# Kernel optimization log

Hardware: AMD Instinct MI355X
Metric: run time of the kernel (lower is better)

## Reference

```python
import jax, jax.numpy as jnp
import numpy as np

B, M, K = 4096, 64, 3          # graphs, points per graph, knn k
FX, FP = 59, 3                 # node features, position dims (FX+FP = 62)
EPS = 1e-5


def _lin_init(key, fan_in, fan_out):
    k1, k2 = jax.random.split(key)
    s = 1.0 / np.sqrt(fan_in)
    W = jax.random.uniform(k1, (fan_in, fan_out), jnp.float32, -s, s)
    b = jax.random.uniform(k2, (fan_out,), jnp.float32, -s, s)
    return W, b


def setup_inputs() -> dict:
    key = jax.random.key(0)
    ks = jax.random.split(key, 8)
    x = jax.random.normal(ks[0], (B * M, FX), jnp.float32)
    pos = jax.random.normal(ks[1], (B * M, FP), jnp.float32)
    batch = jnp.repeat(jnp.arange(B, dtype=jnp.int32), M)
    W1, b1 = _lin_init(ks[2], FX + FP, 128)
    W2, b2 = _lin_init(ks[3], 128, 128)
    Wc1, bc1 = _lin_init(ks[4], 128, 256)
    Wc2, bc2 = _lin_init(ks[5], 256, 1)
    return dict(
        x=x, pos=pos, batch=batch,
        W1=W1, b1=b1, g1=jnp.ones(128), be1=jnp.zeros(128),
        W2=W2, b2=b2, g2=jnp.ones(128), be2=jnp.zeros(128),
        Wc1=Wc1, bc1=bc1, gc1=jnp.ones(256), bec1=jnp.zeros(256),
        Wc2=Wc2, bc2=bc2, gc2=jnp.ones(1), bec2=jnp.zeros(1),
    )


def _mlp_block(h, W, b, g, be):
    # Linear -> ReLU -> BatchNorm1d (training-mode batch statistics)
    h = jax.nn.relu(h @ W + b)
    mu = h.mean(axis=0)
    var = h.var(axis=0)  # biased, as torch BN uses for normalization
    return g * (h - mu) * jax.lax.rsqrt(var + EPS) + be


def _knn_idx(pos_b):
    # pos_b: [B, M, FP]; per-graph k-NN (loop=False)
    d = jnp.sum((pos_b[:, :, None, :] - pos_b[:, None, :, :]) ** 2, axis=-1)  # [B,M,M]
    d = d + jnp.eye(M, dtype=d.dtype) * 1e10  # exclude self-loops
    _, nbr = jax.lax.top_k(-d, K)  # [B, M, K] neighbor (source) indices
    return nbr


def reference(x, pos, batch, W1, b1, g1, be1, W2, b2, g2, be2,
              Wc1, bc1, gc1, bec1, Wc2, bc2, gc2, bec2):
    x_b = x.reshape(B, M, FX)
    pos_b = pos.reshape(B, M, FP)
    nbr = _knn_idx(pos_b)                                   # [B,M,K]
    # gather neighbor features and relative positions (edge messages)
    xj = jax.vmap(lambda xb, nb: xb[nb])(x_b, nbr)          # [B,M,K,FX]
    pj = jax.vmap(lambda pb, nb: pb[nb])(pos_b, nbr)        # [B,M,K,FP]
    rel = pj - pos_b[:, :, None, :]
    msg = jnp.concatenate([xj, rel], axis=-1).reshape(B * M * K, FX + FP)
    # local_nn on every edge, then max aggregation per target node
    h = _mlp_block(msg, W1, b1, g1, be1)                    # [E,128]
    h = h.reshape(B, M, K, 128).max(axis=2).reshape(B * M, 128)
    # global_nn per node
    h = _mlp_block(h, W2, b2, g2, be2)                      # [N,128]
    # global mean pool over graphs
    sums = jax.ops.segment_sum(h, batch, num_segments=B)
    cnt = jax.ops.segment_sum(jnp.ones((B * M,), h.dtype), batch, num_segments=B)
    pooled = sums / cnt[:, None]                            # [B,128]
    # classifier MLP([128,256,1])
    c = _mlp_block(pooled, Wc1, bc1, gc1, bec1)
    c = _mlp_block(c, Wc2, bc2, gc2, bec2)                  # [B,1]
    return jax.nn.sigmoid(c)[:, 0]
```

## Files before the change

### kernel.cpp

```cpp
#include <hip/hip_runtime.h>
#include <hip/hip_bf16.h>
#include <math.h>

#define NB   4096
#define MM   64
#define KNN  3
#define FX   59
#define H    128
#define NN   (NB*MM)
#define NE   (NN*KNN)
#define C1   256
#define EPSB 1e-5f

typedef __attribute__((ext_vector_type(8))) short short8;
typedef __attribute__((ext_vector_type(4))) float f32x4;

__device__ __forceinline__ float wave_red(float v) {
#pragma unroll
    for (int m = 32; m >= 1; m >>= 1) v += __shfl_xor(v, m, 64);
    return v;
}

__device__ __forceinline__ unsigned short f2bf(float f) {
    union { float f; unsigned u; } v; v.f = f;
    unsigned r = v.u + 0x7fffu + ((v.u >> 16) & 1u);
    return (unsigned short)(r >> 16);
}

__device__ __forceinline__ unsigned int pack_bf2(float a, float b) {
    union { __hip_bfloat162 h; unsigned int u; } cv;
    cv.h = __float22bfloat162_rn(make_float2(a, b));
    return cv.u;
}

__global__ __launch_bounds__(128) void k_prep2(
    const float* __restrict__ W2, const float* __restrict__ affine1,
    const float* __restrict__ b2, unsigned short* __restrict__ W2t,
    float* __restrict__ b2p)
{
    const int n = blockIdx.x, k = threadIdx.x;
    float wv = W2[k * H + n];
    W2t[n * H + k] = f2bf(affine1[k] * wv);
    float contrib = wave_red(affine1[H + k] * wv);
    __shared__ float red2[2];
    if ((k & 63) == 0) red2[k >> 6] = contrib;
    __syncthreads();
    if (k == 0) b2p[n] = b2[n] + red2[0] + red2[1];
}

__global__ __launch_bounds__(512, 8) void k_knn_mfma1(
    const float* __restrict__ x, const float* __restrict__ pos,
    const float* __restrict__ W1, const float* __restrict__ b1,
    unsigned short* __restrict__ h1max, float* __restrict__ p1s,
    float* __restrict__ p1q)
{
    __shared__ float pos_s[MM * 3];
    __shared__ int   nbr_s[MM * 3];
    __shared__ float b1_s[H];
    __shared__ float w1p_s[3 * H];
    __shared__ __align__(16) unsigned short a_s[MM * 72];
    __shared__ __align__(16) unsigned int   u_s32[MM * 66];

    const int blk = blockIdx.x, tid = threadIdx.x;
    const float* xg = x + (size_t)blk * MM * FX;
    const float* pg = pos + (size_t)blk * MM * 3;

    {
        const int node = tid >> 3, c0g = (tid & 7) * 8;
        unsigned short vals[8];
#pragma unroll
        for (int i = 0; i < 8; ++i) {
            int c = c0g + i;
            float v = (c < FX) ? xg[node * FX + c]
                               : ((c < 62) ? pg[node * 3 + (c - FX)] : 0.f);
            vals[i] = f2bf(v);
        }
        *(short8*)(a_s + node * 72 + c0g) = *(short8*)&vals[0];
    }
    if (tid < MM * 3) pos_s[tid] = pg[tid];
    if (tid < H) b1_s[tid] = b1[tid];
    if (tid < 3 * H) w1p_s[tid] = W1[(FX + (tid >> 7)) * H + (tid & 127)];

    const int lane = tid & 63;
    const int w    = tid >> 6;
    const int m    = lane & 15;
    const int kg   = lane >> 4;
    const int ch   = w * 16 + m;

    short8 bfr[2];
#pragma unroll
    for (int kc = 0; kc < 2; ++kc) {
        unsigned short t8[8];
#pragma unroll
        for (int i = 0; i < 8; ++i) {
            int k = kc * 32 + kg * 8 + i;
            t8[i] = (k < 62) ? f2bf(W1[k * H + ch]) : (unsigned short)0;
        }
        bfr[kc] = *(short8*)t8;
    }
    __syncthreads();

    {
        const int node = tid >> 3, q = tid & 7;
        const float px = pos_s[node * 3 + 0];
        const float py = pos_s[node * 3 + 1];
        const float pz = pos_s[node * 3 + 2];
        float d0 = 1e30f, d1 = 1e30f, d2 = 1e30f;
        int   i0 = 1 << 30, i1 = 1 << 30, i2 = 1 << 30;
        for (int jj = 0; jj < 8; ++jj) {
            int j = q * 8 + jj;
            if (j == node) continue;
            float dx = pos_s[j * 3 + 0] - px;
            float dy = pos_s[j * 3 + 1] - py;
            float dz = pos_s[j * 3 + 2] - pz;
            float d = dx * dx + dy * dy + dz * dz;
            bool b2v = (d < d2) || (d == d2 && j < i2);
            bool b1v = (d < d1) || (d == d1 && j < i1);
            bool b0v = (d < d0) || (d == d0 && j < i0);
            float nd2 = b1v ? d1 : d; int ni2 = b1v ? i1 : j;
            float nd1 = b0v ? d0 : d; int ni1 = b0v ? i0 : j;
            d2 = b2v ? nd2 : d2; i2 = b2v ? ni2 : i2;
            d1 = b1v ? nd1 : d1; i1 = b1v ? ni1 : i1;
            d0 = b0v ? d   : d0; i0 = b0v ? j   : i0;
        }
#pragma unroll
        for (int mq = 1; mq <= 4; mq <<= 1) {
            float e[3]; int f[3];
            e[0] = __shfl_xor(d0, mq, 64); f[0] = __shfl_xor(i0, mq, 64);
            e[1] = __shfl_xor(d1, mq, 64); f[1] = __shfl_xor(i1, mq, 64);
            e[2] = __shfl_xor(d2, mq, 64); f[2] = __shfl_xor(i2, mq, 64);
#pragma unroll
            for (int t3 = 0; t3 < 3; ++t3) {
                float ev = e[t3]; int fv = f[t3];
                bool b2v = (ev < d2) || (ev == d2 && fv < i2);
                bool b1v = (ev < d1) || (ev == d1 && fv < i1);
                bool b0v = (ev < d0) || (ev == d0 && fv < i0);
                float nd2 = b1v ? d1 : ev; int ni2 = b1v ? i1 : fv;
                float nd1 = b0v ? d0 : ev; int ni1 = b0v ? i0 : fv;
                d2 = b2v ? nd2 : d2; i2 = b2v ? ni2 : i2;
                d1 = b1v ? nd1 : d1; i1 = b1v ? ni1 : i1;
                d0 = b0v ? ev  : d0; i0 = b0v ? fv  : i0;
            }
        }
        if (q == 0) {
            nbr_s[node * 3 + 0] = i0;
            nbr_s[node * 3 + 1] = i1;
            nbr_s[node * 3 + 2] = i2;
        }
    }

    f32x4 acc[4];
#pragma unroll
    for (int rt = 0; rt < 4; ++rt) acc[rt] = (f32x4){0.f, 0.f, 0.f, 0.f};

#pragma unroll
    for (int kc = 0; kc < 2; ++kc)
#pragma unroll
        for (int rt = 0; rt < 4; ++rt) {
            short8 a = *(const short8*)(a_s + (rt * 16 + m) * 72 + kc * 32 + kg * 8);
            acc[rt] = __builtin_amdgcn_mfma_f32_16x16x32_bf16(bfr[kc], a, acc[rt], 0, 0, 0);
        }
#pragma unroll
    for (int rt = 0; rt < 4; ++rt) {
        int node = rt * 16 + m;
        int pidx = 8 * w + 2 * kg;
        uint2 val;
        val.x = pack_bf2(acc[rt][0], acc[rt][1]);
        val.y = pack_bf2(acc[rt][2], acc[rt][3]);
        *(uint2*)(u_s32 + node * 66 + pidx) = val;
    }
    __syncthreads();

    const int c0 = 2 * lane, c1v = 2 * lane + 1;
    const float wpa0 = w1p_s[c0],      wpa1 = w1p_s[H + c0],  wpa2 = w1p_s[2 * H + c0];
    const float wpb0 = w1p_s[c1v],     wpb1 = w1p_s[H + c1v], wpb2 = w1p_s[2 * H + c1v];
    const float b1a = b1_s[c0], b1b = b1_s[c1v];
    float s0 = 0.f, s1 = 0.f, q0 = 0.f, q1 = 0.f;
    unsigned int* hout32 = (unsigned int*)(h1max + (size_t)blk * MM * H);
#pragma unroll
    for (int ii = 0; ii < 8; ++ii) {
        int node = w * 8 + ii;
        int j0 = nbr_s[node * 3 + 0];
        int j1 = nbr_s[node * 3 + 1];
        int j2 = nbr_s[node * 3 + 2];
        float px = pos_s[node * 3 + 0], py = pos_s[node * 3 + 1], pz = pos_s[node * 3 + 2];
        float basea = b1a - (px * wpa0 + py * wpa1 + pz * wpa2);
        float baseb = b1b - (px * wpb0 + py * wpb1 + pz * wpb2);
        unsigned int v0 = u_s32[j0 * 66 + lane];
        unsigned int v1 = u_s32[j1 * 66 + lane];
        unsigned int v2 = u_s32[j2 * 66 + lane];
        float h0a = fmaxf(__uint_as_float(v0 << 16) + basea, 0.f);
        float h1a = fmaxf(__uint_as_float(v1 << 16) + basea, 0.f);
        float h2a = fmaxf(__uint_as_float(v2 << 16) + basea, 0.f);
        float h0b = fmaxf(__uint_as_float(v0 & 0xffff0000u) + baseb, 0.f);
        float h1b = fmaxf(__uint_as_float(v1 & 0xffff0000u) + baseb, 0.f);
        float h2b = fmaxf(__uint_as_float(v2 & 0xffff0000u) + baseb, 0.f);
        s0 += h0a + h1a + h2a; q0 += h0a * h0a + h1a * h1a + h2a * h2a;
        s1 += h0b + h1b + h2b; q1 += h0b * h0b + h1b * h1b + h2b * h2b;
        float ma = fmaxf(fmaxf(h0a, h1a), h2a);
        float mb = fmaxf(fmaxf(h0b, h1b), h2b);
        hout32[node * 64 + lane] = pack_bf2(ma, mb);
    }
    __syncthreads();

    float* s_red = (float*)a_s;
    float* q_red = (float*)u_s32;
    *(float2*)(s_red + w * 128 + c0) = make_float2(s0, s1);
    *(float2*)(q_red + w * 128 + c0) = make_float2(q0, q1);
    __syncthreads();
    if (tid < 128) {
        float S = 0.f;
#pragma unroll
        for (int ww = 0; ww < 8; ++ww) S += s_red[ww * 128 + tid];
        p1s[(size_t)blk * H + tid] = S;
    } else if (tid < 256) {
        int t2 = tid - 128;
        float Q = 0.f;
#pragma unroll
        for (int ww = 0; ww < 8; ++ww) Q += q_red[ww * 128 + t2];
        p1q[(size_t)blk * H + t2] = Q;
    }
}

__global__ __launch_bounds__(256) void k_stats(
    const float* __restrict__ ps, const float* __restrict__ pq, int P, int ld,
    float invCnt, const float* __restrict__ g, const float* __restrict__ be,
    float* __restrict__ affine, int C)
{
    const int c = blockIdx.x, tid = threadIdx.x;
    float s = 0.f, q = 0.f;
    for (int p = tid; p < P; p += 256) {
        s += ps[(size_t)p * ld + c];
        q += pq[(size_t)p * ld + c];
    }
    s = wave_red(s); q = wave_red(q);
    __shared__ float rs_s[4], rq_s[4];
    if ((tid & 63) == 0) { rs_s[tid >> 6] = s; rq_s[tid >> 6] = q; }
    __syncthreads();
    if (tid == 0) {
        float S = rs_s[0] + rs_s[1] + rs_s[2] + rs_s[3];
        float Q = rq_s[0] + rq_s[1] + rq_s[2] + rq_s[3];
        float mu  = S * invCnt;
        float var = Q * invCnt - mu * mu;
        float a   = g[c] * rsqrtf(var + EPSB);
        affine[c]     = a;
        affine[C + c] = be[c] - mu * a;
    }
}

__global__ __launch_bounds__(256) void k_mfma2(
    const unsigned short* __restrict__ h1max, const unsigned short* __restrict__ W2t,
    const float* __restrict__ b2p,
    float* __restrict__ graphsum, float* __restrict__ p2q)
{
    const int blk = blockIdx.x, tid = threadIdx.x;
    const unsigned short* hg = h1max + (size_t)blk * MM * H;
    const int lane = tid & 63, w = tid >> 6, wcol = w * 32;
    const int m = lane & 15, kg = lane >> 4;

    short8 bfr[2][4];
#pragma unroll
    for (int ct = 0; ct < 2; ++ct)
#pragma unroll
        for (int kc = 0; kc < 4; ++kc)
            bfr[ct][kc] = *(const short8*)(W2t + (wcol + ct * 16 + m) * H + kc * 32 + kg * 8);

    f32x4 acc[4][2];
#pragma unroll
    for (int rt = 0; rt < 4; ++rt)
#pragma unroll
        for (int ct = 0; ct < 2; ++ct) acc[rt][ct] = (f32x4){0.f, 0.f, 0.f, 0.f};

#pragma unroll
    for (int kc = 0; kc < 4; ++kc)
#pragma unroll
        for (int rt = 0; rt < 4; ++rt) {
            short8 a = *(const short8*)(hg + (rt * 16 + m) * H + kc * 32 + kg * 8);
#pragma unroll
            for (int ct = 0; ct < 2; ++ct)
                acc[rt][ct] = __builtin_amdgcn_mfma_f32_16x16x32_bf16(a, bfr[ct][kc], acc[rt][ct], 0, 0, 0);
        }

#pragma unroll
    for (int ct = 0; ct < 2; ++ct) {
        float bv = b2p[wcol + ct * 16 + m];
        float s = 0.f, q = 0.f;
#pragma unroll
        for (int rt = 0; rt < 4; ++rt)
#pragma unroll
            for (int r = 0; r < 4; ++r) {
                float v = fmaxf(acc[rt][ct][r] + bv, 0.f);
                s += v; q += v * v;
            }
        s += __shfl_xor(s, 16, 64); q += __shfl_xor(q, 16, 64);
        s += __shfl_xor(s, 32, 64); q += __shfl_xor(q, 32, 64);
        if (lane < 16) {
            int col = wcol + ct * 16 + lane;
            graphsum[(size_t)blk * H + col] = s;
            p2q[(size_t)blk * H + col] = q;
        }
    }
}

__global__ __launch_bounds__(256) void k_cls1(
    const float* __restrict__ graphsum, const float* __restrict__ affine2,
    const float* __restrict__ Wc1, const float* __restrict__ bc1,
    float* __restrict__ c1raw, float* __restrict__ p3s, float* __restrict__ p3q)
{
    __shared__ float pooled_s[16 * H];
    const int blk = blockIdx.x, tid = threadIdx.x;
    const int g0 = blk * 16;
    for (int t = tid; t < 16 * H; t += 256) {
        int f = t & 127;
        pooled_s[t] = affine2[f] * (graphsum[(size_t)g0 * H + t] * (1.f / 64.f)) + affine2[H + f];
    }
    __syncthreads();
    const int c = tid;
    float acc[16];
    const float bias = bc1[c];
#pragma unroll
    for (int gi = 0; gi < 16; ++gi) acc[gi] = bias;
    for (int f = 0; f < H; ++f) {
        float w = Wc1[f * C1 + c];
#pragma unroll
        for (int gi = 0; gi < 16; ++gi) acc[gi] += pooled_s[gi * H + f] * w;
    }
    float s = 0.f, q = 0.f;
#pragma unroll
    for (int gi = 0; gi < 16; ++gi) {
        float h = fmaxf(acc[gi], 0.f);
        c1raw[(size_t)(g0 + gi) * C1 + c] = h;
        s += h; q += h * h;
    }
    p3s[(size_t)blk * C1 + c] = s;
    p3q[(size_t)blk * C1 + c] = q;
}

__global__ __launch_bounds__(256) void k_cls2(
    const float* __restrict__ c1raw, const float* __restrict__ affine3,
    const float* __restrict__ Wc2, const float* __restrict__ bc2,
    float* __restrict__ z, float* __restrict__ pz, float* __restrict__ pzq)
{
    __shared__ float a_s[C1], c_s[C1], w_s[C1];
    const int blk = blockIdx.x, tid = threadIdx.x;
    a_s[tid] = affine3[tid];
    c_s[tid] = affine3[C1 + tid];
    w_s[tid] = Wc2[tid];
    __syncthreads();
    const int g = blk * 256 + tid;
    float acc = bc2[0];
    for (int f = 0; f < C1; f += 4) {
        float4 cv = *(const float4*)&c1raw[(size_t)g * C1 + f];
        acc += (a_s[f + 0] * cv.x + c_s[f + 0]) * w_s[f + 0];
        acc += (a_s[f + 1] * cv.y + c_s[f + 1]) * w_s[f + 1];
        acc += (a_s[f + 2] * cv.z + c_s[f + 2]) * w_s[f + 2];
        acc += (a_s[f + 3] * cv.w + c_s[f + 3]) * w_s[f + 3];
    }
    float zz = fmaxf(acc, 0.f);
    z[g] = zz;
    float s = wave_red(zz);
    float q = wave_red(zz * zz);
    __shared__ float rs_s[4], rq_s[4];
    if ((tid & 63) == 0) { rs_s[tid >> 6] = s; rq_s[tid >> 6] = q; }
    __syncthreads();
    if (tid == 0) {
        pz[blk]  = rs_s[0] + rs_s[1] + rs_s[2] + rs_s[3];
        pzq[blk] = rq_s[0] + rq_s[1] + rq_s[2] + rq_s[3];
    }
}

__global__ __launch_bounds__(256) void k_final(
    const float* __restrict__ z, const float* __restrict__ pz,
    const float* __restrict__ pzq, const float* __restrict__ gc2,
    const float* __restrict__ bec2, float* __restrict__ out)
{
    __shared__ float ab[2];
    if (threadIdx.x == 0) {
        float S = 0.f, Q = 0.f;
        for (int p = 0; p < 16; ++p) { S += pz[p]; Q += pzq[p]; }
        float mu  = S * (1.f / 4096.f);
        float var = Q * (1.f / 4096.f) - mu * mu;
        float a   = gc2[0] * rsqrtf(var + EPSB);
        ab[0] = a;
        ab[1] = bec2[0] - mu * a;
    }
    __syncthreads();
    float a = ab[0], cb = ab[1];
    for (int g = threadIdx.x; g < NB; g += 256) {
        float v = a * z[g] + cb;
        out[g] = 1.f / (1.f + expf(-v));
    }
}

extern "C" void kernel_launch(void* const* d_in, const int* in_sizes, int n_in,
                              void* d_out, int out_size, void* d_ws, size_t ws_size,
                              hipStream_t stream)
{
    const float* x    = (const float*)d_in[0];
    const float* pos  = (const float*)d_in[1];
    const float* W1   = (const float*)d_in[3];
    const float* b1   = (const float*)d_in[4];
    const float* g1   = (const float*)d_in[5];
    const float* be1  = (const float*)d_in[6];
    const float* W2   = (const float*)d_in[7];
    const float* b2   = (const float*)d_in[8];
    const float* g2   = (const float*)d_in[9];
    const float* be2  = (const float*)d_in[10];
    const float* Wc1  = (const float*)d_in[11];
    const float* bc1  = (const float*)d_in[12];
    const float* gc1  = (const float*)d_in[13];
    const float* bec1 = (const float*)d_in[14];
    const float* Wc2  = (const float*)d_in[15];
    const float* bc2  = (const float*)d_in[16];
    const float* gc2  = (const float*)d_in[17];
    const float* bec2 = (const float*)d_in[18];
    float* out = (float*)d_out;

    float* ws = (float*)d_ws;
    size_t off = 0;
    auto alloc = [&](size_t n) { float* p = ws + off; off += n; return p; };
    unsigned short* h1max = (unsigned short*)alloc((size_t)NN * H / 2);
    unsigned short* W2t   = (unsigned short*)alloc(128 * 128 / 2);
    float* b2p     = alloc(H);
    float* p1s     = alloc((size_t)NB * H);
    float* p1q     = alloc((size_t)NB * H);
    float* affine1 = alloc(2 * H);
    float* graphsum= alloc((size_t)NB * H);
    float* p2q     = alloc((size_t)NB * H);
    float* affine2 = alloc(2 * H);
    float* c1raw   = alloc((size_t)NB * C1);
    float* p3s     = alloc((size_t)256 * C1);
    float* p3q     = alloc((size_t)256 * C1);
    float* affine3 = alloc(2 * C1);
    float* zbuf    = alloc(NB);
    float* pz      = alloc(16);
    float* pzq     = alloc(16);

    k_knn_mfma1<<<dim3(NB), dim3(512), 0, stream>>>(x, pos, W1, b1, h1max, p1s, p1q);
    k_stats<<<dim3(H), dim3(256), 0, stream>>>(p1s, p1q, NB, H, 1.f / (float)NE, g1, be1, affine1, H);
    k_prep2<<<dim3(128), dim3(128), 0, stream>>>(W2, affine1, b2, W2t, b2p);
    k_mfma2<<<dim3(NB), dim3(256), 0, stream>>>(h1max, W2t, b2p, graphsum, p2q);
    k_stats<<<dim3(H), dim3(256), 0, stream>>>(graphsum, p2q, NB, H, 1.f / (float)NN, g2, be2, affine2, H);
    k_cls1<<<dim3(256), dim3(256), 0, stream>>>(graphsum, affine2, Wc1, bc1, c1raw, p3s, p3q);
    k_stats<<<dim3(C1), dim3(256), 0, stream>>>(p3s, p3q, 256, C1, 1.f / (float)NB, gc1, bec1, affine3, C1);
    k_cls2<<<dim3(16), dim3(256), 0, stream>>>(c1raw, affine3, Wc2, bc2, zbuf, pz, pzq);
    k_final<<<dim3(1), dim3(256), 0, stream>>>(zbuf, pz, pzq, gc2, bec2, out);
}
```

Measured before the change: 278.9 us.

## Fuse stats and classifier stages into cooperative kernels with grid sync

Replaces the chain of small kernels (stats, prep2, stats, cls1, stats, cls2, final) with two cooperative kernels that use grid-wide syncs between phases. Column statistics are now reduced by 256 blocks in parallel instead of one block per channel looping over 4096 partials. k_mfma2 also stages its A tile into padded LDS before the MFMA loop. This removes launch gaps and serial reductions, at the cost of grid-sync overhead and cooperative-launch constraints.

Result: slower. 380.9 us (+36.5%).

```diff
diff --git a/kernel.cpp b/kernel.cpp
--- a/kernel.cpp
+++ b/kernel.cpp
@@ -1,6 +1,9 @@
 #include <hip/hip_runtime.h>
 #include <hip/hip_bf16.h>
+#include <hip/hip_cooperative_groups.h>
 #include <math.h>
+
+namespace cg = cooperative_groups;
 
 #define NB   4096
 #define MM   64
@@ -31,21 +34,6 @@
     union { __hip_bfloat162 h; unsigned int u; } cv;
     cv.h = __float22bfloat162_rn(make_float2(a, b));
     return cv.u;
-}
-
-__global__ __launch_bounds__(128) void k_prep2(
-    const float* __restrict__ W2, const float* __restrict__ affine1,
-    const float* __restrict__ b2, unsigned short* __restrict__ W2t,
-    float* __restrict__ b2p)
-{
-    const int n = blockIdx.x, k = threadIdx.x;
-    float wv = W2[k * H + n];
-    W2t[n * H + k] = f2bf(affine1[k] * wv);
-    float contrib = wave_red(affine1[H + k] * wv);
-    __shared__ float red2[2];
-    if ((k & 63) == 0) red2[k >> 6] = contrib;
-    __syncthreads();
-    if (k == 0) b2p[n] = b2[n] + red2[0] + red2[1];
 }
 
 __global__ __launch_bounds__(512, 8) void k_knn_mfma1(
@@ -222,30 +210,59 @@
     }
 }
 
-__global__ __launch_bounds__(256) void k_stats(
-    const float* __restrict__ ps, const float* __restrict__ pq, int P, int ld,
-    float invCnt, const float* __restrict__ g, const float* __restrict__ be,
-    float* __restrict__ affine, int C)
+__global__ __launch_bounds__(256) void k_mid(
+    const float* __restrict__ p1s, const float* __restrict__ p1q,
+    const float* __restrict__ W2, const float* __restrict__ g1,
+    const float* __restrict__ be1, const float* __restrict__ b2,
+    float* __restrict__ pp1s, float* __restrict__ pp1q,
+    unsigned short* __restrict__ W2t, float* __restrict__ b2p)
 {
-    const int c = blockIdx.x, tid = threadIdx.x;
-    float s = 0.f, q = 0.f;
-    for (int p = tid; p < P; p += 256) {
-        s += ps[(size_t)p * ld + c];
-        q += pq[(size_t)p * ld + c];
-    }
-    s = wave_red(s); q = wave_red(q);
-    __shared__ float rs_s[4], rq_s[4];
-    if ((tid & 63) == 0) { rs_s[tid >> 6] = s; rq_s[tid >> 6] = q; }
-    __syncthreads();
-    if (tid == 0) {
-        float S = rs_s[0] + rs_s[1] + rs_s[2] + rs_s[3];
-        float Q = rq_s[0] + rq_s[1] + rq_s[2] + rq_s[3];
-        float mu  = S * invCnt;
-        float var = Q * invCnt - mu * mu;
-        float a   = g[c] * rsqrtf(var + EPSB);
-        affine[c]     = a;
-        affine[C + c] = be[c] - mu * a;
-    }
+    const int b = blockIdx.x, tid = threadIdx.x;
+    {
+        const int cgp = b & 7, pc = b >> 3;
+        const int m = tid & 15, r = tid >> 4;
+        const int c = cgp * 16 + m;
+        float s = 0.f, q = 0.f;
+#pragma unroll
+        for (int i = 0; i < 8; ++i) {
+            int p = pc * 128 + r + i * 16;
+            s += p1s[(size_t)p * H + c];
+            q += p1q[(size_t)p * H + c];
+        }
+        s += __shfl_xor(s, 16, 64); s += __shfl_xor(s, 32, 64);
+        q += __shfl_xor(q, 16, 64); q += __shfl_xor(q, 32, 64);
+        __shared__ float rs[4][16], rq[4][16];
+        const int w = tid >> 6, lane = tid & 63;
+        if (lane < 16) { rs[w][lane] = s; rq[w][lane] = q; }
+        __syncthreads();
+        if (tid < 16)
+            pp1s[pc * H + cgp * 16 + tid] = rs[0][tid] + rs[1][tid] + rs[2][tid] + rs[3][tid];
+        else if (tid < 32) {
+            int t = tid - 16;
+            pp1q[pc * H + cgp * 16 + t] = rq[0][t] + rq[1][t] + rq[2][t] + rq[3][t];
+        }
+    }
+    cg::this_grid().sync();
+    if (b >= H) return;
+    const int n = b, k = tid;
+    float contrib = 0.f;
+    if (k < H) {
+        float S = 0.f, Q = 0.f;
+#pragma unroll 8
+        for (int p = 0; p < 32; ++p) { S += pp1s[p * H + k]; Q += pp1q[p * H + k]; }
+        float mu  = S * (1.f / (float)NE);
+        float var = Q * (1.f / (float)NE) - mu * mu;
+        float a   = g1[k] * rsqrtf(var + EPSB);
+        float cc  = be1[k] - mu * a;
+        float wv  = W2[k * H + n];
+        W2t[n * H + k] = f2bf(a * wv);
+        contrib = cc * wv;
+    }
+    contrib = wave_red(contrib);
+    __shared__ float red2[4];
+    if ((tid & 63) == 0) red2[tid >> 6] = contrib;
+    __syncthreads();
+    if (tid == 0) b2p[n] = b2[n] + red2[0] + red2[1] + red2[2] + red2[3];
 }
 
 __global__ __launch_bounds__(256) void k_mfma2(
@@ -253,8 +270,15 @@
     const float* __restrict__ b2p,
     float* __restrict__ graphsum, float* __restrict__ p2q)
 {
+    __shared__ __align__(16) unsigned short a_s[MM * 136];
     const int blk = blockIdx.x, tid = threadIdx.x;
     const unsigned short* hg = h1max + (size_t)blk * MM * H;
+    for (int t = tid; t < MM * H / 8; t += 256) {
+        int row = t >> 4, col8 = (t & 15) * 8;
+        *(short8*)(a_s + row * 136 + col8) = *(const short8*)(hg + row * H + col8);
+    }
+    __syncthreads();
+
     const int lane = tid & 63, w = tid >> 6, wcol = w * 32;
     const int m = lane & 15, kg = lane >> 4;
 
@@ -275,7 +299,7 @@
     for (int kc = 0; kc < 4; ++kc)
 #pragma unroll
         for (int rt = 0; rt < 4; ++rt) {
-            short8 a = *(const short8*)(hg + (rt * 16 + m) * H + kc * 32 + kg * 8);
+            short8 a = *(const short8*)(a_s + (rt * 16 + m) * 136 + kc * 32 + kg * 8);
 #pragma unroll
             for (int ct = 0; ct < 2; ++ct)
                 acc[rt][ct] = __builtin_amdgcn_mfma_f32_16x16x32_bf16(a, bfr[ct][kc], acc[rt][ct], 0, 0, 0);
@@ -302,93 +326,160 @@
     }
 }
 
-__global__ __launch_bounds__(256) void k_cls1(
-    const float* __restrict__ graphsum, const float* __restrict__ affine2,
+__global__ __launch_bounds__(256) void k_tail(
+    const float* __restrict__ graphsum, const float* __restrict__ p2q,
+    const float* __restrict__ g2, const float* __restrict__ be2,
     const float* __restrict__ Wc1, const float* __restrict__ bc1,
-    float* __restrict__ c1raw, float* __restrict__ p3s, float* __restrict__ p3q)
+    const float* __restrict__ gc1, const float* __restrict__ bec1,
+    const float* __restrict__ Wc2, const float* __restrict__ bc2,
+    const float* __restrict__ gc2, const float* __restrict__ bec2,
+    float* __restrict__ pp2s, float* __restrict__ pp2q,
+    float* __restrict__ c1raw, float* __restrict__ p3s, float* __restrict__ p3q,
+    float* __restrict__ affine3, float* __restrict__ pzs, float* __restrict__ pzq,
+    float* __restrict__ out)
 {
+    const int b = blockIdx.x, tid = threadIdx.x;
+
+    {
+        const int cgp = b & 7, pc = b >> 3;
+        const int m = tid & 15, r = tid >> 4;
+        const int c = cgp * 16 + m;
+        float s = 0.f, q = 0.f;
+#pragma unroll
+        for (int i = 0; i < 8; ++i) {
+            int p = pc * 128 + r + i * 16;
+            s += graphsum[(size_t)p * H + c];
+            q += p2q[(size_t)p * H + c];
+        }
+        s += __shfl_xor(s, 16, 64); s += __shfl_xor(s, 32, 64);
+        q += __shfl_xor(q, 16, 64); q += __shfl_xor(q, 32, 64);
+        __shared__ float rs[4][16], rq[4][16];
+        const int w = tid >> 6, lane = tid & 63;
+        if (lane < 16) { rs[w][lane] = s; rq[w][lane] = q; }
+        __syncthreads();
+        if (tid < 16)
+            pp2s[pc * H + cgp * 16 + tid] = rs[0][tid] + rs[1][tid] + rs[2][tid] + rs[3][tid];
+        else if (tid < 32) {
+            int t = tid - 16;
+            pp2q[pc * H + cgp * 16 + t] = rq[0][t] + rq[1][t] + rq[2][t] + rq[3][t];
+        }
+    }
+    cg::this_grid().sync();
+
+    __shared__ float a2_s[H], c2_s[H];
+    if (tid < H) {
+        float S = 0.f, Q = 0.f;
+#pragma unroll 8
+        for (int p = 0; p < 32; ++p) { S += pp2s[p * H + tid]; Q += pp2q[p * H + tid]; }
+        float mu  = S * (1.f / (float)NN);
+        float var = Q * (1.f / (float)NN) - mu * mu;
+        float a   = g2[tid] * rsqrtf(var + EPSB);
+        a2_s[tid] = a;
+        c2_s[tid] = be2[tid] - mu * a;
+    }
+    __syncthreads();
     __shared__ float pooled_s[16 * H];
-    const int blk = blockIdx.x, tid = threadIdx.x;
-    const int g0 = blk * 16;
+    const int g0 = b * 16;
     for (int t = tid; t < 16 * H; t += 256) {
         int f = t & 127;
-        pooled_s[t] = affine2[f] * (graphsum[(size_t)g0 * H + t] * (1.f / 64.f)) + affine2[H + f];
-    }
-    __syncthreads();
-    const int c = tid;
-    float acc[16];
-    const float bias = bc1[c];
-#pragma unroll
-    for (int gi = 0; gi < 16; ++gi) acc[gi] = bias;
-    for (int f = 0; f < H; ++f) {
-        float w = Wc1[f * C1 + c];
-#pragma unroll
-        for (int gi = 0; gi < 16; ++gi) acc[gi] += pooled_s[gi * H + f] * w;
-    }
-    float s = 0.f, q = 0.f;
-#pragma unroll
-    for (int gi = 0; gi < 16; ++gi) {
-        float h = fmaxf(acc[gi], 0.f);
-        c1raw[(size_t)(g0 + gi) * C1 + c] = h;
-        s += h; q += h * h;
-    }
-    p3s[(size_t)blk * C1 + c] = s;
-    p3q[(size_t)blk * C1 + c] = q;
-}
-
-__global__ __launch_bounds__(256) void k_cls2(
-    const float* __restrict__ c1raw, const float* __restrict__ affine3,
-    const float* __restrict__ Wc2, const float* __restrict__ bc2,
-    float* __restrict__ z, float* __restrict__ pz, float* __restrict__ pzq)
-{
-    __shared__ float a_s[C1], c_s[C1], w_s[C1];
-    const int blk = blockIdx.x, tid = threadIdx.x;
-    a_s[tid] = affine3[tid];
-    c_s[tid] = affine3[C1 + tid];
-    w_s[tid] = Wc2[tid];
-    __syncthreads();
-    const int g = blk * 256 + tid;
-    float acc = bc2[0];
-    for (int f = 0; f < C1; f += 4) {
-        float4 cv = *(const float4*)&c1raw[(size_t)g * C1 + f];
-        acc += (a_s[f + 0] * cv.x + c_s[f + 0]) * w_s[f + 0];
-        acc += (a_s[f + 1] * cv.y + c_s[f + 1]) * w_s[f + 1];
-        acc += (a_s[f + 2] * cv.z + c_s[f + 2]) * w_s[f + 2];
-        acc += (a_s[f + 3] * cv.w + c_s[f + 3]) * w_s[f + 3];
-    }
-    float zz = fmaxf(acc, 0.f);
-    z[g] = zz;
-    float s = wave_red(zz);
-    float q = wave_red(zz * zz);
-    __shared__ float rs_s[4], rq_s[4];
-    if ((tid & 63) == 0) { rs_s[tid >> 6] = s; rq_s[tid >> 6] = q; }
+        pooled_s[t] = a2_s[f] * (graphsum[(size_t)g0 * H + t] * (1.f / 64.f)) + c2_s[f];
+    }
+    __syncthreads();
+    {
+        const int c = tid;
+        float acc[16];
+        const float bias = bc1[c];
+#pragma unroll
+        for (int gi = 0; gi < 16; ++gi) acc[gi] = bias;
+        for (int f = 0; f < H; ++f) {
+            float wv = Wc1[f * C1 + c];
+#pragma unroll
+            for (int gi = 0; gi < 16; ++gi) acc[gi] += pooled_s[gi * H + f] * wv;
+        }
+        float s = 0.f, q = 0.f;
+#pragma unroll
+        for (int gi = 0; gi < 16; ++gi) {
+            float h = fmaxf(acc[gi], 0.f);
+            c1raw[(size_t)(g0 + gi) * C1 + c] = h;
+            s += h; q += h * h;
+        }
+        p3s[(size_t)b * C1 + c] = s;
+        p3q[(size_t)b * C1 + c] = q;
+    }
+    cg::this_grid().sync();
+
+    {
+        float s = p3s[(size_t)tid * C1 + b];
+        float q = p3q[(size_t)tid * C1 + b];
+        s = wave_red(s); q = wave_red(q);
+        __shared__ float rs2[4], rq2[4];
+        if ((tid & 63) == 0) { rs2[tid >> 6] = s; rq2[tid >> 6] = q; }
+        __syncthreads();
+        if (tid == 0) {
+            float S = rs2[0] + rs2[1] + rs2[2] + rs2[3];
+            float Q = rq2[0] + rq2[1] + rq2[2] + rq2[3];
+            float mu  = S * (1.f / (float)NB);
+            float var = Q * (1.f / (float)NB) - mu * mu;
+            float a   = gc1[b] * rsqrtf(var + EPSB);
+            affine3[b]      = a;
+            affine3[C1 + b] = bec1[b] - mu * a;
+        }
+    }
+    cg::this_grid().sync();
+
+    __shared__ float a3_s[C1], c3_s[C1], w3_s[C1];
+    __shared__ float zloc[16];
+    a3_s[tid] = affine3[tid];
+    c3_s[tid] = affine3[C1 + tid];
+    w3_s[tid] = Wc2[tid];
+    __syncthreads();
+    {
+        const int gi = tid >> 4, part = tid & 15;
+        const int g = g0 + gi;
+        const float* crow = c1raw + (size_t)g * C1 + part * 16;
+        float acc3 = 0.f;
+#pragma unroll
+        for (int i = 0; i < 16; i += 4) {
+            float4 cv = *(const float4*)(crow + i);
+            int f = part * 16 + i;
+            acc3 += (a3_s[f + 0] * cv.x + c3_s[f + 0]) * w3_s[f + 0];
+            acc3 += (a3_s[f + 1] * cv.y + c3_s[f + 1]) * w3_s[f + 1];
+            acc3 += (a3_s[f + 2] * cv.z + c3_s[f + 2]) * w3_s[f + 2];
+            acc3 += (a3_s[f + 3] * cv.w + c3_s[f + 3]) * w3_s[f + 3];
+        }
+#pragma unroll
+        for (int mm = 1; mm <= 8; mm <<= 1) acc3 += __shfl_xor(acc3, mm, 64);
+        if (part == 0) zloc[gi] = fmaxf(acc3 + bc2[0], 0.f);
+    }
     __syncthreads();
     if (tid == 0) {
-        pz[blk]  = rs_s[0] + rs_s[1] + rs_s[2] + rs_s[3];
-        pzq[blk] = rq_s[0] + rq_s[1] + rq_s[2] + rq_s[3];
-    }
-}
-
-__global__ __launch_bounds__(256) void k_final(
-    const float* __restrict__ z, const float* __restrict__ pz,
-    const float* __restrict__ pzq, const float* __restrict__ gc2,
-    const float* __restrict__ bec2, float* __restrict__ out)
-{
-    __shared__ float ab[2];
-    if (threadIdx.x == 0) {
-        float S = 0.f, Q = 0.f;
-        for (int p = 0; p < 16; ++p) { S += pz[p]; Q += pzq[p]; }
-        float mu  = S * (1.f / 4096.f);
-        float var = Q * (1.f / 4096.f) - mu * mu;
-        float a   = gc2[0] * rsqrtf(var + EPSB);
-        ab[0] = a;
-        ab[1] = bec2[0] - mu * a;
-    }
-    __syncthreads();
-    float a = ab[0], cb = ab[1];
-    for (int g = threadIdx.x; g < NB; g += 256) {
-        float v = a * z[g] + cb;
-        out[g] = 1.f / (1.f + expf(-v));
+        float s = 0.f, q = 0.f;
+#pragma unroll
+        for (int i = 0; i < 16; ++i) { float z = zloc[i]; s += z; q += z * z; }
+        pzs[b] = s; pzq[b] = q;
+    }
+    cg::this_grid().sync();
+
+    {
+        float s = pzs[tid], q = pzq[tid];
+        s = wave_red(s); q = wave_red(q);
+        __shared__ float rs4[4], rq4[4], ab[2];
+        if ((tid & 63) == 0) { rs4[tid >> 6] = s; rq4[tid >> 6] = q; }
+        __syncthreads();
+        if (tid == 0) {
+            float S = rs4[0] + rs4[1] + rs4[2] + rs4[3];
+            float Q = rq4[0] + rq4[1] + rq4[2] + rq4[3];
+            float mu  = S * (1.f / (float)NB);
+            float var = Q * (1.f / (float)NB) - mu * mu;
+            float a   = gc2[0] * rsqrtf(var + EPSB);
+            ab[0] = a;
+            ab[1] = bec2[0] - mu * a;
+        }
+        __syncthreads();
+        if (tid < 16) {
+            float v = ab[0] * zloc[tid] + ab[1];
+            out[g0 + tid] = 1.f / (1.f + expf(-v));
+        }
     }
 }
 
@@ -424,25 +515,33 @@
     float* b2p     = alloc(H);
     float* p1s     = alloc((size_t)NB * H);
     float* p1q     = alloc((size_t)NB * H);
-    float* affine1 = alloc(2 * H);
+    float* pp1s    = alloc(32 * H);
+    float* pp1q    = alloc(32 * H);
     float* graphsum= alloc((size_t)NB * H);
     float* p2q     = alloc((size_t)NB * H);
-    float* affine2 = alloc(2 * H);
+    float* pp2s    = alloc(32 * H);
+    float* pp2q    = alloc(32 * H);
     float* c1raw   = alloc((size_t)NB * C1);
     float* p3s     = alloc((size_t)256 * C1);
     float* p3q     = alloc((size_t)256 * C1);
     float* affine3 = alloc(2 * C1);
-    float* zbuf    = alloc(NB);
-    float* pz      = alloc(16);
-    float* pzq     = alloc(16);
+    float* pzs     = alloc(256);
+    float* pzq     = alloc(256);
 
     k_knn_mfma1<<<dim3(NB), dim3(512), 0, stream>>>(x, pos, W1, b1, h1max, p1s, p1q);
-    k_stats<<<dim3(H), dim3(256), 0, stream>>>(p1s, p1q, NB, H, 1.f / (float)NE, g1, be1, affine1, H);
-    k_prep2<<<dim3(128), dim3(128), 0, stream>>>(W2, affine1, b2, W2t, b2p);
+
+    void* amid[] = { (void*)&p1s, (void*)&p1q, (void*)&W2, (void*)&g1,
+                     (void*)&be1, (void*)&b2, (void*)&pp1s, (void*)&pp1q,
+                     (void*)&W2t, (void*)&b2p };
+    hipLaunchCooperativeKernel(k_mid, dim3(256), dim3(256), amid, 0, stream);
+
     k_mfma2<<<dim3(NB), dim3(256), 0, stream>>>(h1max, W2t, b2p, graphsum, p2q);
-    k_stats<<<dim3(H), dim3(256), 0, stream>>>(graphsum, p2q, NB, H, 1.f / (float)NN, g2, be2, affine2, H);
-    k_cls1<<<dim3(256), dim3(256), 0, stream>>>(graphsum, affine2, Wc1, bc1, c1raw, p3s, p3q);
-    k_stats<<<dim3(C1), dim3(256), 0, stream>>>(p3s, p3q, 256, C1, 1.f / (float)NB, gc1, bec1, affine3, C1);
-    k_cls2<<<dim3(16), dim3(256), 0, stream>>>(c1raw, affine3, Wc2, bc2, zbuf, pz, pzq);
-    k_final<<<dim3(1), dim3(256), 0, stream>>>(zbuf, pz, pzq, gc2, bec2, out);
-}
+
+    void* atail[] = { (void*)&graphsum, (void*)&p2q, (void*)&g2, (void*)&be2,
+                      (void*)&Wc1, (void*)&bc1, (void*)&gc1, (void*)&bec1,
+                      (void*)&Wc2, (void*)&bc2, (void*)&gc2, (void*)&bec2,
+                      (void*)&pp2s, (void*)&pp2q, (void*)&c1raw, (void*)&p3s,
+                      (void*)&p3q, (void*)&affine3, (void*)&pzs, (void*)&pzq,
+                      (void*)&out };
+    hipLaunchCooperativeKernel(k_tail, dim3(256), dim3(256), atail, 0, stream);
+}
```

## Replace per-block BN partial buffers and stats kernels with sharded atomic accumulation

Applied to the files above, without the earlier changes.

Batch-norm sum and sum-of-squares partials are now accumulated with relaxed float atomics into 16-way sharded buffers instead of per-block arrays. Each consumer kernel derives the affine parameters itself, which removes the three k_stats launches and their large partial-buffer reads. k_mfma2 now stages its A tile through padded LDS, and k_cls2 and k_final are re-gridded to use more blocks. The changes add a memset, atomic contention, and nondeterministic summation order in exchange for fewer launches and less memory traffic.

Result: faster. 241.0 us (-13.6%).

```diff
diff --git a/kernel.cpp b/kernel.cpp
--- a/kernel.cpp
+++ b/kernel.cpp
@@ -11,6 +11,7 @@
 #define NE   (NN*KNN)
 #define C1   256
 #define EPSB 1e-5f
+#define NSH  16
 
 typedef __attribute__((ext_vector_type(8))) short short8;
 typedef __attribute__((ext_vector_type(4))) float f32x4;
@@ -19,6 +20,10 @@
 #pragma unroll
     for (int m = 32; m >= 1; m >>= 1) v += __shfl_xor(v, m, 64);
     return v;
+}
+
+__device__ __forceinline__ void atomAddF(float* p, float v) {
+    __hip_atomic_fetch_add(p, v, __ATOMIC_RELAXED, __HIP_MEMORY_SCOPE_AGENT);
 }
 
 __device__ __forceinline__ unsigned short f2bf(float f) {
@@ -33,26 +38,11 @@
     return cv.u;
 }
 
-__global__ __launch_bounds__(128) void k_prep2(
-    const float* __restrict__ W2, const float* __restrict__ affine1,
-    const float* __restrict__ b2, unsigned short* __restrict__ W2t,
-    float* __restrict__ b2p)
-{
-    const int n = blockIdx.x, k = threadIdx.x;
-    float wv = W2[k * H + n];
-    W2t[n * H + k] = f2bf(affine1[k] * wv);
-    float contrib = wave_red(affine1[H + k] * wv);
-    __shared__ float red2[2];
-    if ((k & 63) == 0) red2[k >> 6] = contrib;
-    __syncthreads();
-    if (k == 0) b2p[n] = b2[n] + red2[0] + red2[1];
-}
-
 __global__ __launch_bounds__(512, 8) void k_knn_mfma1(
     const float* __restrict__ x, const float* __restrict__ pos,
     const float* __restrict__ W1, const float* __restrict__ b1,
-    unsigned short* __restrict__ h1max, float* __restrict__ p1s,
-    float* __restrict__ p1q)
+    unsigned short* __restrict__ h1max,
+    float* __restrict__ S1sh, float* __restrict__ Q1sh)
 {
     __shared__ float pos_s[MM * 3];
     __shared__ int   nbr_s[MM * 3];
@@ -208,53 +198,58 @@
     *(float2*)(s_red + w * 128 + c0) = make_float2(s0, s1);
     *(float2*)(q_red + w * 128 + c0) = make_float2(q0, q1);
     __syncthreads();
+    const int sel = blk & (NSH - 1);
     if (tid < 128) {
         float S = 0.f;
 #pragma unroll
         for (int ww = 0; ww < 8; ++ww) S += s_red[ww * 128 + tid];
-        p1s[(size_t)blk * H + tid] = S;
+        atomAddF(&S1sh[sel * H + tid], S);
     } else if (tid < 256) {
         int t2 = tid - 128;
         float Q = 0.f;
 #pragma unroll
         for (int ww = 0; ww < 8; ++ww) Q += q_red[ww * 128 + t2];
-        p1q[(size_t)blk * H + t2] = Q;
-    }
-}
-
-__global__ __launch_bounds__(256) void k_stats(
-    const float* __restrict__ ps, const float* __restrict__ pq, int P, int ld,
-    float invCnt, const float* __restrict__ g, const float* __restrict__ be,
-    float* __restrict__ affine, int C)
-{
-    const int c = blockIdx.x, tid = threadIdx.x;
-    float s = 0.f, q = 0.f;
-    for (int p = tid; p < P; p += 256) {
-        s += ps[(size_t)p * ld + c];
-        q += pq[(size_t)p * ld + c];
-    }
-    s = wave_red(s); q = wave_red(q);
-    __shared__ float rs_s[4], rq_s[4];
-    if ((tid & 63) == 0) { rs_s[tid >> 6] = s; rq_s[tid >> 6] = q; }
-    __syncthreads();
-    if (tid == 0) {
-        float S = rs_s[0] + rs_s[1] + rs_s[2] + rs_s[3];
-        float Q = rq_s[0] + rq_s[1] + rq_s[2] + rq_s[3];
-        float mu  = S * invCnt;
-        float var = Q * invCnt - mu * mu;
-        float a   = g[c] * rsqrtf(var + EPSB);
-        affine[c]     = a;
-        affine[C + c] = be[c] - mu * a;
-    }
+        atomAddF(&Q1sh[sel * H + t2], Q);
+    }
+}
+
+__global__ __launch_bounds__(128) void k_prep2(
+    const float* __restrict__ W2, const float* __restrict__ S1sh,
+    const float* __restrict__ Q1sh, const float* __restrict__ g1,
+    const float* __restrict__ be1, const float* __restrict__ b2,
+    unsigned short* __restrict__ W2t, float* __restrict__ b2p)
+{
+    const int n = blockIdx.x, k = threadIdx.x;
+    float S = 0.f, Q = 0.f;
+#pragma unroll
+    for (int i = 0; i < NSH; ++i) { S += S1sh[i * H + k]; Q += Q1sh[i * H + k]; }
+    float mu  = S * (1.f / (float)NE);
+    float var = Q * (1.f / (float)NE) - mu * mu;
+    float a   = g1[k] * rsqrtf(var + EPSB);
+    float cc  = be1[k] - mu * a;
+    float wv  = W2[k * H + n];
+    W2t[n * H + k] = f2bf(a * wv);
+    float contrib = wave_red(cc * wv);
+    __shared__ float red2[2];
+    if ((k & 63) == 0) red2[k >> 6] = contrib;
+    __syncthreads();
+    if (k == 0) b2p[n] = b2[n] + red2[0] + red2[1];
 }
 
 __global__ __launch_bounds__(256) void k_mfma2(
     const unsigned short* __restrict__ h1max, const unsigned short* __restrict__ W2t,
     const float* __restrict__ b2p,
-    float* __restrict__ graphsum, float* __restrict__ p2q)
-{
+    float* __restrict__ graphsum, float* __restrict__ S2sh, float* __restrict__ Q2sh)
+{
+    __shared__ __align__(16) unsigned short a_s[MM * 136];
     const int blk = blockIdx.x, tid = threadIdx.x;
     const unsigned short* hg = h1max + (size_t)blk * MM * H;
+    for (int t = tid; t < MM * H / 8; t += 256) {
+        int row = t >> 4, col8 = (t & 15) * 8;
+        *(short8*)(a_s + row * 136 + col8) = *(const short8*)(hg + row * H + col8);
+    }
+    __syncthreads();
+
     const int lane = tid & 63, w = tid >> 6, wcol = w * 32;
     const int m = lane & 15, kg = lane >> 4;
 
@@ -275,12 +270,13 @@
     for (int kc = 0; kc < 4; ++kc)
 #pragma unroll
         for (int rt = 0; rt < 4; ++rt) {
-            short8 a = *(const short8*)(hg + (rt * 16 + m) * H + kc * 32 + kg * 8);
+            short8 a = *(const short8*)(a_s + (rt * 16 + m) * 136 + kc * 32 + kg * 8);
 #pragma unroll
             for (int ct = 0; ct < 2; ++ct)
                 acc[rt][ct] = __builtin_amdgcn_mfma_f32_16x16x32_bf16(a, bfr[ct][kc], acc[rt][ct], 0, 0, 0);
         }
 
+    const int sel = blk & (NSH - 1);
 #pragma unroll
     for (int ct = 0; ct < 2; ++ct) {
         float bv = b2p[wcol + ct * 16 + m];
@@ -297,22 +293,37 @@
         if (lane < 16) {
             int col = wcol + ct * 16 + lane;
             graphsum[(size_t)blk * H + col] = s;
-            p2q[(size_t)blk * H + col] = q;
+            atomAddF(&S2sh[sel * H + col], s);
+            atomAddF(&Q2sh[sel * H + col], q);
         }
     }
 }
 
 __global__ __launch_bounds__(256) void k_cls1(
-    const float* __restrict__ graphsum, const float* __restrict__ affine2,
+    const float* __restrict__ graphsum,
+    const float* __restrict__ S2sh, const float* __restrict__ Q2sh,
+    const float* __restrict__ g2, const float* __restrict__ be2,
     const float* __restrict__ Wc1, const float* __restrict__ bc1,
-    float* __restrict__ c1raw, float* __restrict__ p3s, float* __restrict__ p3q)
-{
+    float* __restrict__ c1raw, float* __restrict__ S3, float* __restrict__ Q3)
+{
+    __shared__ float a2_s[H], c2_s[H];
+    const int blk = blockIdx.x, tid = threadIdx.x;
+    if (tid < H) {
+        float S = 0.f, Q = 0.f;
+#pragma unroll
+        for (int i = 0; i < NSH; ++i) { S += S2sh[i * H + tid]; Q += Q2sh[i * H + tid]; }
+        float mu  = S * (1.f / (float)NN);
+        float var = Q * (1.f / (float)NN) - mu * mu;
+        float a   = g2[tid] * rsqrtf(var + EPSB);
+        a2_s[tid] = a;
+        c2_s[tid] = be2[tid] - mu * a;
+    }
+    __syncthreads();
     __shared__ float pooled_s[16 * H];
-    const int blk = blockIdx.x, tid = threadIdx.x;
     const int g0 = blk * 16;
     for (int t = tid; t < 16 * H; t += 256) {
         int f = t & 127;
-        pooled_s[t] = affine2[f] * (graphsum[(size_t)g0 * H + t] * (1.f / 64.f)) + affine2[H + f];
+        pooled_s[t] = a2_s[f] * (graphsum[(size_t)g0 * H + t] * (1.f / 64.f)) + c2_s[f];
     }
     __syncthreads();
     const int c = tid;
@@ -321,9 +332,9 @@
 #pragma unroll
     for (int gi = 0; gi < 16; ++gi) acc[gi] = bias;
     for (int f = 0; f < H; ++f) {
-        float w = Wc1[f * C1 + c];
-#pragma unroll
-        for (int gi = 0; gi < 16; ++gi) acc[gi] += pooled_s[gi * H + f] * w;
+        float wv = Wc1[f * C1 + c];
+#pragma unroll
+        for (int gi = 0; gi < 16; ++gi) acc[gi] += pooled_s[gi * H + f] * wv;
     }
     float s = 0.f, q = 0.f;
 #pragma unroll
@@ -332,64 +343,72 @@
         c1raw[(size_t)(g0 + gi) * C1 + c] = h;
         s += h; q += h * h;
     }
-    p3s[(size_t)blk * C1 + c] = s;
-    p3q[(size_t)blk * C1 + c] = q;
+    atomAddF(&S3[c], s);
+    atomAddF(&Q3[c], q);
 }
 
 __global__ __launch_bounds__(256) void k_cls2(
-    const float* __restrict__ c1raw, const float* __restrict__ affine3,
+    const float* __restrict__ c1raw,
+    const float* __restrict__ S3, const float* __restrict__ Q3,
+    const float* __restrict__ gc1, const float* __restrict__ bec1,
     const float* __restrict__ Wc2, const float* __restrict__ bc2,
-    float* __restrict__ z, float* __restrict__ pz, float* __restrict__ pzq)
-{
-    __shared__ float a_s[C1], c_s[C1], w_s[C1];
+    float* __restrict__ z, float* __restrict__ SzQz)
+{
+    __shared__ float a3_s[C1], c3_s[C1], w3_s[C1];
+    __shared__ float zloc[16];
     const int blk = blockIdx.x, tid = threadIdx.x;
-    a_s[tid] = affine3[tid];
-    c_s[tid] = affine3[C1 + tid];
-    w_s[tid] = Wc2[tid];
-    __syncthreads();
-    const int g = blk * 256 + tid;
-    float acc = bc2[0];
-    for (int f = 0; f < C1; f += 4) {
-        float4 cv = *(const float4*)&c1raw[(size_t)g * C1 + f];
-        acc += (a_s[f + 0] * cv.x + c_s[f + 0]) * w_s[f + 0];
-        acc += (a_s[f + 1] * cv.y + c_s[f + 1]) * w_s[f + 1];
-        acc += (a_s[f + 2] * cv.z + c_s[f + 2]) * w_s[f + 2];
-        acc += (a_s[f + 3] * cv.w + c_s[f + 3]) * w_s[f + 3];
-    }
-    float zz = fmaxf(acc, 0.f);
-    z[g] = zz;
-    float s = wave_red(zz);
-    float q = wave_red(zz * zz);
-    __shared__ float rs_s[4], rq_s[4];
-    if ((tid & 63) == 0) { rs_s[tid >> 6] = s; rq_s[tid >> 6] = q; }
-    __syncthreads();
+    {
+        float S = S3[tid], Q = Q3[tid];
+        float mu  = S * (1.f / (float)NB);
+        float var = Q * (1.f / (float)NB) - mu * mu;
+        float a   = gc1[tid] * rsqrtf(var + EPSB);
+        a3_s[tid] = a;
+        c3_s[tid] = bec1[tid] - mu * a;
+        w3_s[tid] = Wc2[tid];
+    }
+    __syncthreads();
+    const int g0 = blk * 16;
+    {
+        const int gi = tid >> 4, part = tid & 15;
+        const float* crow = c1raw + (size_t)(g0 + gi) * C1 + part * 16;
+        float acc3 = 0.f;
+#pragma unroll
+        for (int i = 0; i < 16; i += 4) {
+            float4 cv = *(const float4*)(crow + i);
+            int f = part * 16 + i;
+            acc3 += (a3_s[f + 0] * cv.x + c3_s[f + 0]) * w3_s[f + 0];
+            acc3 += (a3_s[f + 1] * cv.y + c3_s[f + 1]) * w3_s[f + 1];
+            acc3 += (a3_s[f + 2] * cv.z + c3_s[f + 2]) * w3_s[f + 2];
+            acc3 += (a3_s[f + 3] * cv.w + c3_s[f + 3]) * w3_s[f + 3];
+        }
+#pragma unroll
+        for (int mm = 1; mm <= 8; mm <<= 1) acc3 += __shfl_xor(acc3, mm, 64);
+        if (part == 0) zloc[gi] = fmaxf(acc3 + bc2[0], 0.f);
+    }
+    __syncthreads();
+    if (tid < 16) z[g0 + tid] = zloc[tid];
     if (tid == 0) {
-        pz[blk]  = rs_s[0] + rs_s[1] + rs_s[2] + rs_s[3];
-        pzq[blk] = rq_s[0] + rq_s[1] + rq_s[2] + rq_s[3];
+        float s = 0.f, q = 0.f;
+#pragma unroll
+        for (int i = 0; i < 16; ++i) { float zz = zloc[i]; s += zz; q += zz * zz; }
+        atomAddF(&SzQz[0], s);
+        atomAddF(&SzQz[1], q);
     }
 }
 
 __global__ __launch_bounds__(256) void k_final(
-    const float* __restrict__ z, const float* __restrict__ pz,
-    const float* __restrict__ pzq, const float* __restrict__ gc2,
-    const float* __restrict__ bec2, float* __restrict__ out)
-{
-    __shared__ float ab[2];
-    if (threadIdx.x == 0) {
-        float S = 0.f, Q = 0.f;
-        for (int p = 0; p < 16; ++p) { S += pz[p]; Q += pzq[p]; }
-        float mu  = S * (1.f / 4096.f);
-        float var = Q * (1.f / 4096.f) - mu * mu;
-        float a   = gc2[0] * rsqrtf(var + EPSB);
-        ab[0] = a;
-        ab[1] = bec2[0] - mu * a;
-    }
-    __syncthreads();
-    float a = ab[0], cb = ab[1];
-    for (int g = threadIdx.x; g < NB; g += 256) {
-        float v = a * z[g] + cb;
-        out[g] = 1.f / (1.f + expf(-v));
-    }
+    const float* __restrict__ z, const float* __restrict__ SzQz,
+    const float* __restrict__ gc2, const float* __restrict__ bec2,
+    float* __restrict__ out)
+{
+    const int g = blockIdx.x * 256 + threadIdx.x;
+    float S = SzQz[0], Q = SzQz[1];
+    float mu  = S * (1.f / 4096.f);
+    float var = Q * (1.f / 4096.f) - mu * mu;
+    float a   = gc2[0] * rsqrtf(var + EPSB);
+    float cb  = bec2[0] - mu * a;
+    float v = a * z[g] + cb;
+    out[g] = 1.f / (1.f + expf(-v));
 }
 
 extern "C" void kernel_launch(void* const* d_in, const int* in_sizes, int n_in,
@@ -422,27 +441,24 @@
     unsigned short* h1max = (unsigned short*)alloc((size_t)NN * H / 2);
     unsigned short* W2t   = (unsigned short*)alloc(128 * 128 / 2);
     float* b2p     = alloc(H);
-    float* p1s     = alloc((size_t)NB * H);
-    float* p1q     = alloc((size_t)NB * H);
-    float* affine1 = alloc(2 * H);
     float* graphsum= alloc((size_t)NB * H);
-    float* p2q     = alloc((size_t)NB * H);
-    float* affine2 = alloc(2 * H);
     float* c1raw   = alloc((size_t)NB * C1);
-    float* p3s     = alloc((size_t)256 * C1);
-    float* p3q     = alloc((size_t)256 * C1);
-    float* affine3 = alloc(2 * C1);
     float* zbuf    = alloc(NB);
-    float* pz      = alloc(16);
-    float* pzq     = alloc(16);
-
-    k_knn_mfma1<<<dim3(NB), dim3(512), 0, stream>>>(x, pos, W1, b1, h1max, p1s, p1q);
-    k_stats<<<dim3(H), dim3(256), 0, stream>>>(p1s, p1q, NB, H, 1.f / (float)NE, g1, be1, affine1, H);
-    k_prep2<<<dim3(128), dim3(128), 0, stream>>>(W2, affine1, b2, W2t, b2p);
-    k_mfma2<<<dim3(NB), dim3(256), 0, stream>>>(h1max, W2t, b2p, graphsum, p2q);
-    k_stats<<<dim3(H), dim3(256), 0, stream>>>(graphsum, p2q, NB, H, 1.f / (float)NN, g2, be2, affine2, H);
-    k_cls1<<<dim3(256), dim3(256), 0, stream>>>(graphsum, affine2, Wc1, bc1, c1raw, p3s, p3q);
-    k_stats<<<dim3(C1), dim3(256), 0, stream>>>(p3s, p3q, 256, C1, 1.f / (float)NB, gc1, bec1, affine3, C1);
-    k_cls2<<<dim3(16), dim3(256), 0, stream>>>(c1raw, affine3, Wc2, bc2, zbuf, pz, pzq);
-    k_final<<<dim3(1), dim3(256), 0, stream>>>(zbuf, pz, pzq, gc2, bec2, out);
-}
+    const size_t ATOMN = (size_t)4 * NSH * H + 2 * C1 + 2;
+    float* atomics = alloc(ATOMN);
+    float* S1sh = atomics;
+    float* Q1sh = S1sh + NSH * H;
+    float* S2sh = Q1sh + NSH * H;
+    float* Q2sh = S2sh + NSH * H;
+    float* S3   = Q2sh + NSH * H;
+    float* Q3   = S3 + C1;
+    float* SzQz = Q3 + C1;
+
+    hipMemsetAsync(atomics, 0, ATOMN * sizeof(float), stream);
+    k_knn_mfma1<<<dim3(NB), dim3(512), 0, stream>>>(x, pos, W1, b1, h1max, S1sh, Q1sh);
+    k_prep2<<<dim3(128), dim3(128), 0, stream>>>(W2, S1sh, Q1sh, g1, be1, b2, W2t, b2p);
+    k_mfma2<<<dim3(NB), dim3(256), 0, stream>>>(h1max, W2t, b2p, graphsum, S2sh, Q2sh);
+    k_cls1<<<dim3(256), dim3(256), 0, stream>>>(graphsum, S2sh, Q2sh, g2, be2, Wc1, bc1, c1raw, S3, Q3);
+    k_cls2<<<dim3(256), dim3(256), 0, stream>>>(c1raw, S3, Q3, gc1, bec1, Wc2, bc2, zbuf, SzQz);
+    k_final<<<dim3(16), dim3(256), 0, stream>>>(zbuf, SzQz, gc2, bec2, out);
+}
```
